# Performance work log

Hardware: AMD Instinct MI355X
Metric: run time of the kernel (lower is better)

Reference implementation:

```python
import jax, jax.numpy as jnp
import numpy as np

# ---- constants matching the torch module / entmax normmax_bisect defaults ----
ALPHA = 5.0                 # normmax alpha (entmax normmax_bisect default)
N_BISECT = 50               # bisection iterations
K_EXP = 1.0 / (ALPHA - 1.0)        # p_i propto (z_i - tau)_+^{1/(alpha-1)}
AK_EXP = ALPHA / (ALPHA - 1.0)     # norm condition: sum (z-tau)_+^{alpha/(alpha-1)} = 1
EPS = 1e-8                  # module epsilon
LN_EPS = 1e-5               # torch LayerNorm default eps

B, N, C, D = 32, 1024, 64, 768


def _bisect_tau(z):
    # z: [..., S]; find tau with f(tau) = sum_i relu(z_i - tau)^AK_EXP - 1 = 0 (f decreasing)
    max_val = jnp.max(z, axis=-1, keepdims=True)
    lo, hi = max_val - 1.0, max_val  # f(lo) >= 0, f(hi) = -1 < 0

    def body(_, carry):
        lo, hi = carry
        tau = 0.5 * (lo + hi)
        f = jnp.sum(jnp.maximum(z - tau, 0.0) ** AK_EXP, axis=-1, keepdims=True) - 1.0
        lo = jnp.where(f >= 0, tau, lo)
        hi = jnp.where(f >= 0, hi, tau)
        return (lo, hi)

    lo, hi = jax.lax.fori_loop(0, N_BISECT, body, (lo, hi))
    return 0.5 * (lo + hi)


def normmax_last(z):
    # normmax over last axis: p = s / sum(s), s = relu(z - tau)^{1/(alpha-1)}, ||s||_alpha = 1
    tau = _bisect_tau(z)
    u = jnp.maximum(z - tau, 0.0)
    u_safe = jnp.where(u > 0, u, 1.0)
    s = jnp.where(u > 0, u_safe ** K_EXP, 0.0)
    return s / jnp.sum(s, axis=-1, keepdims=True)


def layernorm(x, scale, bias):
    mu = jnp.mean(x, axis=-1, keepdims=True)
    var = jnp.mean((x - mu) ** 2, axis=-1, keepdims=True)
    return (x - mu) * jax.lax.rsqrt(var + LN_EPS) * scale + bias


def setup_inputs() -> dict:
    key = jax.random.key(0)
    ks = jax.random.split(key, 10)
    w = lambda k, shp: (jax.random.normal(k, shp, dtype=jnp.float32) * 0.02)
    return {
        "features": jax.random.normal(ks[0], (B, N, D), dtype=jnp.float32),
        "slots_init": jax.random.normal(ks[1], (B, C, D), dtype=jnp.float32),
        "mask": jax.random.randint(ks[2], (B, N), 0, 2, dtype=jnp.int32),
        "ln_f_scale": jnp.ones((D,), jnp.float32),
        "ln_f_bias": jnp.zeros((D,), jnp.float32),
        "ln_s_scale": jnp.ones((D,), jnp.float32),
        "ln_s_bias": jnp.zeros((D,), jnp.float32),
        "Wk": w(ks[3], (D, D)),
        "Wv": w(ks[4], (D, D)),
        "Wq": w(ks[5], (D, D)),
        "W_ih": w(ks[6], (3 * D, D)),
        "W_hh": w(ks[7], (3 * D, D)),
        "b_ih": jnp.zeros((3 * D,), jnp.float32),
        "b_hh": jnp.zeros((3 * D,), jnp.float32),
    }


def reference(features, slots_init, mask, ln_f_scale, ln_f_bias, ln_s_scale, ln_s_bias,
              Wk, Wv, Wq, W_ih, W_hh, b_ih, b_hh):
    f = layernorm(features, ln_f_scale, ln_f_bias)        # [B,N,D]
    k = f @ Wk.T
    v = f @ Wv.T
    b, n, d = v.shape
    c = slots_init.shape[1]
    m = mask[:, None, :] != 0                             # [B,1,N], broadcasts over C

    # num_iterations = 1; straight-through (detach trick) is the identity here.
    slots_prev = slots_init
    s = layernorm(slots_init, ln_s_scale, ln_s_bias)
    q = s @ Wq.T                                          # [B,C,D]
    logits = jnp.einsum('bcd,bnd->bcn', q, k) * (1.0 / np.sqrt(d))
    logits = jnp.where(m, logits, 0.0)                    # masked_fill(mask==0, 0)
    # normmax over the slot axis (dim=1)
    attn = jnp.moveaxis(normmax_last(jnp.moveaxis(logits, 1, -1)), -1, 1)  # [B,C,N]
    attn = jnp.where(m, attn, 0.0)
    attn_wm = attn / (jnp.sum(attn, axis=-1, keepdims=True) + EPS)
    updates = jnp.einsum('bcn,bnd->bcd', attn_wm, v)      # [B,C,D]

    # torch GRUCell: r,z,n gate order
    x = updates.reshape(-1, d)
    h = slots_prev.reshape(-1, d)
    gi = x @ W_ih.T + b_ih
    gh = h @ W_hh.T + b_hh
    ir, iz, in_ = jnp.split(gi, 3, axis=-1)
    hr, hz, hn = jnp.split(gh, 3, axis=-1)
    r = jax.nn.sigmoid(ir + hr)
    zg = jax.nn.sigmoid(iz + hz)
    ng = jnp.tanh(in_ + r * hn)
    h_new = (1.0 - zg) * ng + zg * h
    slots = h_new.reshape(b, c, d)
    return slots, attn
```

## Files before the change

kernel.cpp:

```cpp
#include <hip/hip_runtime.h>
#include <cstdint>
#include <cmath>

#define DEVINL __device__ __forceinline__


using f32x4  = __attribute__((ext_vector_type(4))) float;
using bf16x8 = __attribute__((ext_vector_type(8))) __bf16;
using u16x8  = __attribute__((ext_vector_type(8))) unsigned short;
using u16x4  = __attribute__((ext_vector_type(4))) unsigned short;
using fl4    = __attribute__((ext_vector_type(4))) float;

DEVINL float bf2f(unsigned short h) {
    unsigned int u = ((unsigned int)h) << 16;
    float f; __builtin_memcpy(&f, &u, 4); return f;
}
DEVINL unsigned short f2bf(float f) {
    unsigned int u; __builtin_memcpy(&u, &f, 4);
    u += 0x7FFFu + ((u >> 16) & 1u);
    return (unsigned short)(u >> 16);
}
DEVINL float sqrt_raw(float x) {
    float r; asm("v_sqrt_f32 %0, %1" : "=v"(r) : "v"(x)); return r;
}

DEVINL void gload_lds16(const unsigned short* g, unsigned short* l) {
    __builtin_amdgcn_global_load_lds(
        (__attribute__((address_space(1))) void*)g,
        (__attribute__((address_space(3))) void*)l,
        16, 0, 0);
}

__global__ __launch_bounds__(256)
void mask_scan(const int* __restrict__ mask, int* __restrict__ idx,
               int* __restrict__ cnt, int* __restrict__ cpad)
{
    constexpr int NB = 1024;
    const int b = blockIdx.x * 4 + (threadIdx.x >> 6);
    const int lane = threadIdx.x & 63;
    if (b >= 32) return;
    const int* mrow = mask + b * NB;
    int loc[16]; int lsum = 0;
#pragma unroll
    for (int i = 0; i < 16; ++i) { loc[i] = mrow[lane * 16 + i] != 0; lsum += loc[i]; }
    int pre = lsum;
#pragma unroll
    for (int o = 1; o < 64; o <<= 1) {
        int t = __shfl_up(pre, o);
        if (lane >= o) pre += t;
    }
    const int total = __shfl(pre, 63);
    pre -= lsum;
    int* ib = idx + b * NB;
    int p = pre;
#pragma unroll
    for (int i = 0; i < 16; ++i) if (loc[i]) ib[p++] = lane * 16 + i;
    if (lane == 0) {
        cnt[b] = total;
        int cp = (total + 63) & ~63;
        cpad[b] = cp < 64 ? 64 : cp;
    }
}

__global__ __launch_bounds__(256)
void zfill(float* __restrict__ p, int n4)
{
    const int i = blockIdx.x * 256 + threadIdx.x;
    if (i < n4) { fl4 z = {0.f, 0.f, 0.f, 0.f}; *(fl4*)(p + i * 4) = z; }
}

__global__ __launch_bounds__(256)
void tr2_f2b_split(const float* __restrict__ Wq, const float* __restrict__ Wk,
                   unsigned short* __restrict__ WqT_i, unsigned short* __restrict__ WkT_i)
{
    constexpr int S = 768 * 768;
    const int o = blockIdx.x * 256 + threadIdx.x;
    if (o >= 2 * S) return;
    const float* x; unsigned short* y; int i;
    if (o < S) { x = Wq; y = WqT_i; i = o; }
    else       { x = Wk; y = WkT_i; i = o - S; }
    const int e = i / 768, d = i - e * 768;
    const float v = x[d * 768 + e];
    const unsigned short h = f2bf(v);
    y[(long)e * 1536 + d]       = h;
    y[(long)e * 1536 + 768 + d] = f2bf(v - bf2f(h));
}

__global__ __launch_bounds__(256)
void conv2_fused(const float* __restrict__ Wih, const float* __restrict__ Whh,
                 const float* __restrict__ sl,  const float* __restrict__ Wv,
                 unsigned short* __restrict__ Wihb, unsigned short* __restrict__ Whhb,
                 unsigned short* __restrict__ slb,  unsigned short* __restrict__ Wvb)
{
    constexpr int S1 = 3 * 768 * 768;
    constexpr int S2 = S1 + 3 * 768 * 768;
    constexpr int S3 = S2 + 32 * 64 * 768;
    constexpr int S4 = S3 + 768 * 768;
    const int i = (blockIdx.x * 256 + threadIdx.x) * 4;
    if (i >= S4) return;
    const float* src; unsigned short* dst; int off;
    if (i < S1)      { src = Wih; dst = Wihb; off = i; }
    else if (i < S2) { src = Whh; dst = Whhb; off = i - S1; }
    else if (i < S3) { src = sl;  dst = slb;  off = i - S2; }
    else             { src = Wv;  dst = Wvb;  off = i - S3; }
    fl4 v = *(const fl4*)(src + off);
    u16x4 o;
#pragma unroll
    for (int j = 0; j < 4; ++j) o[j] = f2bf(v[j]);
    *(u16x4*)(dst + off) = o;
}

template<int BM, int BN, int WAVES_M, int WAVES_N, int OUTMODE>
__global__ __launch_bounds__(256)
void gemm_bt3(const unsigned short* __restrict__ AB, const unsigned short* __restrict__ BB,
              void* __restrict__ out1, const int* __restrict__ cpad,
              int N, int K, long sA, long sB, long sC, float alpha)
{
    constexpr int BK = 32;
    constexpr int WM = BM / WAVES_M, WN = BN / WAVES_N;
    constexpr int MT = WM / 16, NT = WN / 16;
    __shared__ alignas(16) unsigned short Ash[BM * BK], Asl[BM * BK];
    __shared__ alignas(16) unsigned short Bsh[BN * BK], Bsl[BN * BK];

    const int bz = blockIdx.z;
    const int row0 = blockIdx.y * BM, col0 = blockIdx.x * BN;
    if (cpad && col0 >= cpad[bz]) return;
    AB += (long)bz * sA;
    BB += (long)bz * sB;
    const int tid = threadIdx.x, l = tid & 63, w = tid >> 6;
    const int wm = w / WAVES_N, wn = w % WAVES_N;
    const int fr = l & 15, fq = l >> 4;

    f32x4 acc[MT][NT] = {};
    constexpr int ACALLS = (BM * BK) / (256 * 8);
    constexpr int BCALLS = (BN * BK) / (256 * 8);

    for (int kt = 0; kt < K; kt += BK) {
#pragma unroll
        for (int c = 0; c < ACALLS; ++c) {
            const int e = (c * 256 + tid) * 8;
            const long rb = (long)(row0 + (e >> 5)) * (2 * K) + kt + (e & 31);
            gload_lds16(AB + rb, &Ash[e]);
            gload_lds16(AB + rb + K, &Asl[e]);
        }
#pragma unroll
        for (int c = 0; c < BCALLS; ++c) {
            const int e = (c * 256 + tid) * 8;
            const long rb = (long)(col0 + (e >> 5)) * (2 * K) + kt + (e & 31);
            gload_lds16(BB + rb, &Bsh[e]);
            gload_lds16(BB + rb + K, &Bsl[e]);
        }
        __syncthreads();

        bf16x8 afh[MT], afl[MT], bfh[NT], bfl[NT];
#pragma unroll
        for (int m = 0; m < MT; ++m) {
            const int o = (wm * WM + m * 16 + fr) * BK + fq * 8;
            afh[m] = __builtin_bit_cast(bf16x8, *(const u16x8*)&Ash[o]);
            afl[m] = __builtin_bit_cast(bf16x8, *(const u16x8*)&Asl[o]);
        }
#pragma unroll
        for (int n = 0; n < NT; ++n) {
            const int o = (wn * WN + n * 16 + fr) * BK + fq * 8;
            bfh[n] = __builtin_bit_cast(bf16x8, *(const u16x8*)&Bsh[o]);
            bfl[n] = __builtin_bit_cast(bf16x8, *(const u16x8*)&Bsl[o]);
        }
#pragma unroll
        for (int m = 0; m < MT; ++m)
#pragma unroll
            for (int n = 0; n < NT; ++n) {
                acc[m][n] = __builtin_amdgcn_mfma_f32_16x16x32_bf16(afh[m], bfh[n], acc[m][n], 0, 0, 0);
                acc[m][n] = __builtin_amdgcn_mfma_f32_16x16x32_bf16(afh[m], bfl[n], acc[m][n], 0, 0, 0);
                acc[m][n] = __builtin_amdgcn_mfma_f32_16x16x32_bf16(afl[m], bfh[n], acc[m][n], 0, 0, 0);
            }
        __syncthreads();
    }

#pragma unroll
    for (int m = 0; m < MT; ++m) {
        const int gr = row0 + wm * WM + m * 16 + fq * 4;
#pragma unroll
        for (int n = 0; n < NT; ++n) {
            const int gc = col0 + wn * WN + n * 16 + fr;
#pragma unroll
            for (int j = 0; j < 4; ++j) {
                const float v = acc[m][n][j] * alpha;
                if (OUTMODE == 0) {
                    ((float*)out1)[(long)bz * sC + (long)(gr + j) * N + gc] = v;
                } else {
                    unsigned short* ob = (unsigned short*)out1;
                    const long rb = (long)(gr + j) * (2 * N) + gc;
                    const unsigned short h = f2bf(v);
                    ob[rb] = h;
                    ob[rb + N] = f2bf(v - bf2f(h));
                }
            }
        }
    }
}

template<int BM, int BN, int WAVES_M, int WAVES_N, bool OUT_F32>
__global__ __launch_bounds__(256)
void gemm_bt(const unsigned short* __restrict__ A,
             const unsigned short* __restrict__ B,
             void* __restrict__ Cv,
             int N, int K, long sA, long sB, long sC, float alpha)
{
    constexpr int BK = 32;
    constexpr int WM = BM / WAVES_M, WN = BN / WAVES_N;
    constexpr int MT = WM / 16, NT = WN / 16;
    __shared__ alignas(16) unsigned short As[BM * BK];
    __shared__ alignas(16) unsigned short Bs[BN * BK];

    const int bz = blockIdx.z;
    A += (long)bz * sA;
    B += (long)bz * sB;
    const int row0 = blockIdx.y * BM, col0 = blockIdx.x * BN;
    const int tid = threadIdx.x, l = tid & 63, w = tid >> 6;
    const int wm = w / WAVES_N, wn = w % WAVES_N;
    const int fr = l & 15, fq = l >> 4;

    f32x4 acc[MT][NT] = {};
    constexpr int ACALLS = (BM * BK) / (256 * 8);
    constexpr int BCALLS = (BN * BK) / (256 * 8);

    for (int kt = 0; kt < K; kt += BK) {
#pragma unroll
        for (int c = 0; c < ACALLS; ++c) {
            const int e = (c * 256 + tid) * 8;
            gload_lds16(A + (long)(row0 + (e >> 5)) * K + kt + (e & 31), &As[e]);
        }
#pragma unroll
        for (int c = 0; c < BCALLS; ++c) {
            const int e = (c * 256 + tid) * 8;
            gload_lds16(B + (long)(col0 + (e >> 5)) * K + kt + (e & 31), &Bs[e]);
        }
        __syncthreads();

        bf16x8 af[MT], bfr[NT];
#pragma unroll
        for (int m = 0; m < MT; ++m)
            af[m] = __builtin_bit_cast(bf16x8, *(const u16x8*)&As[(wm * WM + m * 16 + fr) * BK + fq * 8]);
#pragma unroll
        for (int n = 0; n < NT; ++n)
            bfr[n] = __builtin_bit_cast(bf16x8, *(const u16x8*)&Bs[(wn * WN + n * 16 + fr) * BK + fq * 8]);
#pragma unroll
        for (int m = 0; m < MT; ++m)
#pragma unroll
            for (int n = 0; n < NT; ++n)
                acc[m][n] = __builtin_amdgcn_mfma_f32_16x16x32_bf16(af[m], bfr[n], acc[m][n], 0, 0, 0);
        __syncthreads();
    }

#pragma unroll
    for (int m = 0; m < MT; ++m) {
        const int gr = row0 + wm * WM + m * 16 + fq * 4;
#pragma unroll
        for (int n = 0; n < NT; ++n) {
            const int gc = col0 + wn * WN + n * 16 + fr;
#pragma unroll
            for (int j = 0; j < 4; ++j) {
                const float v = acc[m][n][j] * alpha;
                if (OUT_F32) ((float*)Cv)[(long)bz * sC + (long)(gr + j) * N + gc] = v;
                else ((unsigned short*)Cv)[(long)bz * sC + (long)(gr + j) * N + gc] = f2bf(v);
            }
        }
    }
}

template<int BM, int BN, int WAVES_M, int WAVES_N>
__global__ __launch_bounds__(256)
void gemm_nt_rs(const unsigned short* __restrict__ A,
                const unsigned short* __restrict__ Bm,
                unsigned short* __restrict__ C,
                const int* __restrict__ cpad,
                int N, int Kmax, long sA, long sB, long sC)
{
    constexpr int BK = 32;
    constexpr int WM = BM / WAVES_M, WN = BN / WAVES_N;
    constexpr int MT = WM / 16, NT = WN / 16;
    __shared__ alignas(16) unsigned short As[BM * BK];
    __shared__ alignas(16) unsigned short Bs[BN * BK];
    __shared__ float rsums[BM];

    const int bz = blockIdx.z;
    const int Keff = cpad[bz];
    A += (long)bz * sA;
    Bm += (long)bz * sB;
    const int row0 = blockIdx.y * BM, col0 = blockIdx.x * BN;
    const int tid = threadIdx.x, l = tid & 63, w = tid >> 6;
    const int wm = w / WAVES_N, wn = w % WAVES_N;
    const int fr = l & 15, fq = l >> 4;

    f32x4 acc[MT][NT] = {};
    float rsum = 0.f;
    constexpr int ACALLS = (BM * BK) / (256 * 8);
    constexpr int TPR = BN / 8;
    constexpr int RPP = 256 / TPR;
    const int br = tid / TPR, bc8 = (tid % TPR) * 8;

    for (int kt = 0; kt < Keff; kt += BK) {
#pragma unroll
        for (int c = 0; c < ACALLS; ++c) {
            const int e = (c * 256 + tid) * 8;
            gload_lds16(A + (long)(row0 + (e >> 5)) * Kmax + kt + (e & 31), &As[e]);
        }
#pragma unroll
        for (int p = 0; p < BK / RPP; ++p) {
            const int r = p * RPP + br;
            u16x8 vv = *(const u16x8*)(Bm + (long)(kt + r) * (2 * N) + col0 + bc8);
#pragma unroll
            for (int j = 0; j < 8; ++j) Bs[(bc8 + j) * BK + r] = vv[j];
        }
        __syncthreads();

        if (tid < BM) {
#pragma unroll
            for (int kk = 0; kk < BK / 8; ++kk) {
                u16x8 vv = *(const u16x8*)&As[tid * BK + kk * 8];
#pragma unroll
                for (int j = 0; j < 8; ++j) rsum += bf2f(vv[j]);
            }
        }

        bf16x8 af[MT], bfr[NT];
#pragma unroll
        for (int m = 0; m < MT; ++m)
            af[m] = __builtin_bit_cast(bf16x8, *(const u16x8*)&As[(wm * WM + m * 16 + fr) * BK + fq * 8]);
#pragma unroll
        for (int n = 0; n < NT; ++n)
            bfr[n] = __builtin_bit_cast(bf16x8, *(const u16x8*)&Bs[(wn * WN + n * 16 + fr) * BK + fq * 8]);
#pragma unroll
        for (int m = 0; m < MT; ++m)
#pragma unroll
            for (int n = 0; n < NT; ++n)
                acc[m][n] = __builtin_amdgcn_mfma_f32_16x16x32_bf16(af[m], bfr[n], acc[m][n], 0, 0, 0);
        __syncthreads();
    }

    if (tid < BM) rsums[tid] = rsum;
    __syncthreads();

#pragma unroll
    for (int m = 0; m < MT; ++m) {
        const int lr = wm * WM + m * 16 + fq * 4;
        const int gr = row0 + lr;
#pragma unroll
        for (int n = 0; n < NT; ++n) {
            const int gc = col0 + wn * WN + n * 16 + fr;
#pragma unroll
            for (int j = 0; j < 4; ++j) {
                const float inv = 1.f / (rsums[lr + j] + 1e-8f);
                C[(long)bz * sC + (long)(gr + j) * N + gc] = f2bf(acc[m][n][j] * inv);
            }
        }
    }
}

__global__ __launch_bounds__(256)
void ln_fused_c(const float* __restrict__ xf, const float* __restrict__ gf,
                const float* __restrict__ bf,
                unsigned short* __restrict__ fi,
                const float* __restrict__ xs, const float* __restrict__ gs,
                const float* __restrict__ bs,
                unsigned short* __restrict__ si,
                const int* __restrict__ idx, const int* __restrict__ cnt,
                const int* __restrict__ cpad, int nrows_f)
{
    constexpr int D = 768;
    const int lane = threadIdx.x & 63;
    long row = (long)blockIdx.x * 4 + (threadIdx.x >> 6);
    const float *x, *g, *bb_;
    unsigned short* y;
    long srow;
    if (row < nrows_f) {
        const int b = (int)(row >> 10), j = (int)(row & 1023);
        if (j >= cpad[b]) return;
        y = fi; srow = row;
        unsigned short* yr = y + srow * (2 * D);
        if (j >= cnt[b]) {
            u16x8 z = {};
            unsigned short* p = yr + lane * 24;
            *(u16x8*)p = z; *(u16x8*)(p + 8) = z; *(u16x8*)(p + 16) = z;
            return;
        }
        const int n = idx[(b << 10) + j];
        x = xf + ((long)(b << 10) + n) * D;
        g = gf; bb_ = bf;
    } else {
        srow = row - nrows_f;
        x = xs + srow * D;
        g = gs; bb_ = bs; y = si;
    }

    const int eA = lane * 8;
    const int eB = 512 + lane * 8;
    float v[16];
    {
        fl4 a = *(const fl4*)(x + eA);
        fl4 b = *(const fl4*)(x + eA + 4);
#pragma unroll
        for (int j = 0; j < 4; ++j) { v[j] = a[j]; v[4 + j] = b[j]; }
    }
    if (lane < 32) {
        fl4 a = *(const fl4*)(x + eB);
        fl4 b = *(const fl4*)(x + eB + 4);
#pragma unroll
        for (int j = 0; j < 4; ++j) { v[8 + j] = a[j]; v[12 + j] = b[j]; }
    }
    float s = 0.f, s2 = 0.f;
#pragma unroll
    for (int j = 0; j < 8; ++j) { s += v[j]; s2 += v[j] * v[j]; }
    if (lane < 32) {
#pragma unroll
        for (int j = 8; j < 16; ++j) { s += v[j]; s2 += v[j] * v[j]; }
    }
#pragma unroll
    for (int o = 1; o < 64; o <<= 1) { s += __shfl_xor(s, o); s2 += __shfl_xor(s2, o); }
    const float mu  = s / (float)D;
    const float var = s2 / (float)D - mu * mu;
    const float r   = rsqrtf(var + 1e-5f);

    unsigned short* yr = (row < nrows_f ? fi : si) + srow * (2 * D);
    {
        fl4 g0 = *(const fl4*)(g + eA), g1 = *(const fl4*)(g + eA + 4);
        fl4 b0 = *(const fl4*)(bb_ + eA), b1 = *(const fl4*)(bb_ + eA + 4);
        u16x8 oh, ol;
#pragma unroll
        for (int j = 0; j < 8; ++j) {
            const float gg = (j < 4) ? g0[j] : g1[j - 4];
            const float be = (j < 4) ? b0[j] : b1[j - 4];
            const float yv = (v[j] - mu) * r * gg + be;
            oh[j] = f2bf(yv);
            ol[j] = f2bf(yv - bf2f(oh[j]));
        }
        *(u16x8*)(yr + eA) = oh;
        *(u16x8*)(yr + D + eA) = ol;
    }
    if (lane < 32) {
        fl4 g0 = *(const fl4*)(g + eB), g1 = *(const fl4*)(g + eB + 4);
        fl4 b0 = *(const fl4*)(bb_ + eB), b1 = *(const fl4*)(bb_ + eB + 4);
        u16x8 oh, ol;
#pragma unroll
        for (int j = 0; j < 8; ++j) {
            const float gg = (j < 4) ? g0[j] : g1[j - 4];
            const float be = (j < 4) ? b0[j] : b1[j - 4];
            const float yv = (v[8 + j] - mu) * r * gg + be;
            oh[j] = f2bf(yv);
            ol[j] = f2bf(yv - bf2f(oh[j]));
        }
        *(u16x8*)(yr + eB) = oh;
        *(u16x8*)(yr + D + eB) = ol;
    }
}

__global__ __launch_bounds__(256)
void normmax_cols_c(const float* __restrict__ logits,
                    const int* __restrict__ idx, const int* __restrict__ cnt,
                    const int* __restrict__ cpad,
                    float* __restrict__ attn_f32, unsigned short* __restrict__ attn_b16)
{
    constexpr int N = 1024, C = 64;
    const int b = blockIdx.y;
    const int j0 = blockIdx.x * 64;
    if (j0 >= cpad[b]) return;
    const int tid = threadIdx.x, l = tid & 63, w = tid >> 6;
    const int j = j0 + w * 16 + (l & 15);
    const int cb = (l >> 4) * 16;
    const long base = (long)b * C * N + j;
    const bool valid = j < cnt[b];

    float z[16];
#pragma unroll
    for (int i = 0; i < 16; ++i) z[i] = valid ? logits[base + (long)(cb + i) * N] : 0.f;

    float mx = z[0];
#pragma unroll
    for (int i = 1; i < 16; ++i) mx = fmaxf(mx, z[i]);
    mx = fmaxf(mx, __shfl_xor(mx, 16));
    mx = fmaxf(mx, __shfl_xor(mx, 32));

    float lo = mx - 1.f, hi = mx;
    for (int it = 0; it < 34; ++it) {
        const float tau = 0.5f * (lo + hi);
        float f = 0.f;
#pragma unroll
        for (int i = 0; i < 16; ++i) {
            const float u = fmaxf(z[i] - tau, 0.f);
            f += u * sqrt_raw(sqrt_raw(u));
        }
        f += __shfl_xor(f, 16);
        f += __shfl_xor(f, 32);
        if (f >= 1.f) lo = tau; else hi = tau;
    }
    const float tau = 0.5f * (lo + hi);
    float sv[16]; float ss = 0.f;
#pragma unroll
    for (int i = 0; i < 16; ++i) {
        const float u = fmaxf(z[i] - tau, 0.f);
        sv[i] = sqrt_raw(sqrt_raw(u));
        ss += sv[i];
    }
    ss += __shfl_xor(ss, 16);
    ss += __shfl_xor(ss, 32);
    const float inv = 1.f / ss;
    const int n = valid ? idx[(b << 10) + j] : 0;
#pragma unroll
    for (int i = 0; i < 16; ++i) {
        const float a = valid ? sv[i] * inv : 0.f;
        attn_b16[base + (long)(cb + i) * N] = f2bf(a);
        if (valid) attn_f32[(long)b * C * N + (long)(cb + i) * N + n] = a;
    }
}

__global__ __launch_bounds__(256)
void gru_gates(const float* __restrict__ gi, const float* __restrict__ gh,
               const float* __restrict__ b_ih, const float* __restrict__ b_hh,
               const float* __restrict__ h, float* __restrict__ out)
{
    constexpr int D = 768;
    const int t = blockIdx.x * 256 + threadIdx.x;
    const int row = t / (D / 4), d = (t - row * (D / 4)) * 4;
    const float* gir = gi + (long)row * 3 * D;
    const float* ghr = gh + (long)row * 3 * D;
    fl4 ir  = *(const fl4*)(gir + d);
    fl4 iz  = *(const fl4*)(gir + D + d);
    fl4 in_ = *(const fl4*)(gir + 2 * D + d);
    fl4 hr  = *(const fl4*)(ghr + d);
    fl4 hz  = *(const fl4*)(ghr + D + d);
    fl4 hn  = *(const fl4*)(ghr + 2 * D + d);
    fl4 bir = *(const fl4*)(b_ih + d);
    fl4 biz = *(const fl4*)(b_ih + D + d);
    fl4 bin = *(const fl4*)(b_ih + 2 * D + d);
    fl4 bhr = *(const fl4*)(b_hh + d);
    fl4 bhz = *(const fl4*)(b_hh + D + d);
    fl4 bhn = *(const fl4*)(b_hh + 2 * D + d);
    fl4 hv  = *(const fl4*)(h + (long)row * D + d);
    fl4 o;
#pragma unroll
    for (int j = 0; j < 4; ++j) {
        const float r  = 1.f / (1.f + expf(-(ir[j] + bir[j] + hr[j] + bhr[j])));
        const float zg = 1.f / (1.f + expf(-(iz[j] + biz[j] + hz[j] + bhz[j])));
        const float ng = tanhf(in_[j] + bin[j] + r * (hn[j] + bhn[j]));
        o[j] = (1.f - zg) * ng + zg * hv[j];
    }
    *(fl4*)(out + (long)row * D + d) = o;
}

extern "C" void kernel_launch(void* const* d_in, const int* in_sizes, int n_in,
                              void* d_out, int out_size, void* d_ws, size_t ws_size,
                              hipStream_t stream)
{
    const float* features = (const float*)d_in[0];
    const float* slots    = (const float*)d_in[1];
    const int*   mask     = (const int*)d_in[2];
    const float* lnf_g = (const float*)d_in[3];
    const float* lnf_b = (const float*)d_in[4];
    const float* lns_g = (const float*)d_in[5];
    const float* lns_b = (const float*)d_in[6];
    const float* Wk  = (const float*)d_in[7];
    const float* Wv  = (const float*)d_in[8];
    const float* Wq  = (const float*)d_in[9];
    const float* Wih = (const float*)d_in[10];
    const float* Whh = (const float*)d_in[11];
    const float* bih = (const float*)d_in[12];
    const float* bhh = (const float*)d_in[13];

    constexpr int B = 32, N = 1024, C = 64, D = 768;
    char* ws = (char*)d_ws;
    unsigned short* f_i  = (unsigned short*)(ws + 0);
    float*          gi   = (float*)(ws + 0);
    float*          gh   = (float*)(ws + 18874368);
    unsigned short* Wihb = (unsigned short*)(ws + 37748736);
    unsigned short* Whhb = (unsigned short*)(ws + 41287680);
    unsigned short* Wvb  = (unsigned short*)(ws + 44826624);
    unsigned short* updb = (unsigned short*)(ws + 57671680);
    unsigned short* slb  = (unsigned short*)(ws + 60817408);
    float*          lg     = (float*)(ws + 100663296);
    unsigned short* s_i    = (unsigned short*)(ws + 109051904);
    unsigned short* ab16   = (unsigned short*)(ws + 109051904);
    unsigned short* qk_i   = (unsigned short*)(ws + 115343360);
    unsigned short* Pbf    = (unsigned short*)(ws + 115343360);
    unsigned short* WqT_i  = (unsigned short*)(ws + 121634816);
    unsigned short* WkT_i  = (unsigned short*)(ws + 123994112);
    unsigned short* M_i    = (unsigned short*)(ws + 126353408);
    int*            idx    = (int*)(ws + 128712704);
    int*            cnt    = (int*)(ws + 128843776);
    int*            cpad   = (int*)(ws + 128843904);

    float* out_slots = (float*)d_out;
    float* out_attn  = out_slots + (long)B * C * D;

    mask_scan<<<8, 256, 0, stream>>>(mask, idx, cnt, cpad);
    zfill<<<(B * C * N / 4 + 255) / 256, 256, 0, stream>>>(out_attn, B * C * N / 4);

    tr2_f2b_split<<<(2 * D * D + 255) / 256, 256, 0, stream>>>(Wq, Wk, WqT_i, WkT_i);

    ln_fused_c<<<(B * N + B * C) / 4, 256, 0, stream>>>(
        features, lnf_g, lnf_b, f_i,
        slots, lns_g, lns_b, s_i,
        idx, cnt, cpad, B * N);

    gemm_bt3<64, 64, 2, 2, 1><<<dim3(D / 64, D / 64, 1), 256, 0, stream>>>(
        WkT_i, WqT_i, M_i, nullptr, D, D, 0, 0, 0, 1.f);
    gemm_bt3<64, 64, 2, 2, 1><<<dim3(D / 64, (B * C) / 64, 1), 256, 0, stream>>>(
        s_i, M_i, qk_i, nullptr, D, D, 0, 0, 0, 1.f);
    gemm_bt3<64, 64, 2, 2, 0><<<dim3(N / 64, 1, B), 256, 0, stream>>>(
        qk_i, f_i, lg, cpad,
        N, D, (long)C * 2 * D, (long)N * 2 * D, (long)C * N, 0.03608439182435161f);

    normmax_cols_c<<<dim3(N / 64, B), 256, 0, stream>>>(lg, idx, cnt, cpad, out_attn, ab16);

    gemm_nt_rs<64, 64, 2, 2><<<dim3(D / 64, 1, B), 256, 0, stream>>>(
        ab16, f_i, Pbf, cpad, D, N, (long)C * N, (long)N * 2 * D, (long)C * D);

    {
        constexpr int TOT = 3 * D * D + 3 * D * D + B * C * D + D * D;
        conv2_fused<<<(TOT / 4 + 255) / 256, 256, 0, stream>>>(
            Wih, Whh, slots, Wv, Wihb, Whhb, slb, Wvb);
    }

    gemm_bt<64, 64, 2, 2, false><<<dim3(D / 64, (B * C) / 64, 1), 256, 0, stream>>>(
        Pbf, Wvb, updb, D, D, 0, 0, 0, 1.f);

    gemm_bt<128, 128, 2, 2, true><<<dim3(3 * D / 128, (B * C) / 128, 2), 256, 0, stream>>>(
        updb, Wihb, gi, 3 * D, D,
        (long)(B * C) * D, (long)(3 * D) * D, (long)(B * C) * 3 * D, 1.f);

    gru_gates<<<(B * C * D / 4) / 256, 256, 0, stream>>>(gi, gh, bih, bhh, slots, out_slots);
}
```

Baseline: 202.4 us.

## Fuse GRU input/hidden GEMMs with gate epilogue; merge mask scan and zero-fill

Replaces the batched GRU GEMM, which wrote gi/gh to fp32 workspace, and the separate gates kernel with one kernel. Each 64x64 output tile computes all three gate projections for both input and hidden paths and applies the GRU nonlinearity in registers. Mask scan and attention zero-fill are also merged into one launch. This removes the large gi/gh round trip through memory and two launches, but the new GEMM is single-buffered with a 64x64 tile and holds many accumulators, which may lower occupancy.

```diff
diff --git a/kernel.cpp b/kernel.cpp
--- a/kernel.cpp
+++ b/kernel.cpp
@@ -32,11 +32,18 @@
 }
 
 __global__ __launch_bounds__(256)
-void mask_scan(const int* __restrict__ mask, int* __restrict__ idx,
-               int* __restrict__ cnt, int* __restrict__ cpad)
-{
+void mask_scan_zfill(const int* __restrict__ mask, int* __restrict__ idx,
+                     int* __restrict__ cnt, int* __restrict__ cpad,
+                     float* __restrict__ zp)
+{
+    if (blockIdx.x < 2048) {
+        const int i = blockIdx.x * 256 + threadIdx.x;
+        fl4 z = {0.f, 0.f, 0.f, 0.f};
+        *(fl4*)(zp + (long)i * 4) = z;
+        return;
+    }
     constexpr int NB = 1024;
-    const int b = blockIdx.x * 4 + (threadIdx.x >> 6);
+    const int b = (blockIdx.x - 2048) * 4 + (threadIdx.x >> 6);
     const int lane = threadIdx.x & 63;
     if (b >= 32) return;
     const int* mrow = mask + b * NB;
@@ -60,13 +67,6 @@
         int cp = (total + 63) & ~63;
         cpad[b] = cp < 64 ? 64 : cp;
     }
-}
-
-__global__ __launch_bounds__(256)
-void zfill(float* __restrict__ p, int n4)
-{
-    const int i = blockIdx.x * 256 + threadIdx.x;
-    if (i < n4) { fl4 z = {0.f, 0.f, 0.f, 0.f}; *(fl4*)(p + i * 4) = z; }
 }
 
 __global__ __launch_bounds__(256)
@@ -268,6 +268,87 @@
     }
 }
 
+__global__ __launch_bounds__(256)
+void gemm_gru(const unsigned short* __restrict__ updb, const unsigned short* __restrict__ slb,
+              const unsigned short* __restrict__ Wihb, const unsigned short* __restrict__ Whhb,
+              const float* __restrict__ b_ih, const float* __restrict__ b_hh,
+              const float* __restrict__ h, float* __restrict__ out)
+{
+    constexpr int BK = 32, Kd = 768, Dd = 768;
+    __shared__ alignas(16) unsigned short Au[64 * BK], As[64 * BK];
+    __shared__ alignas(16) unsigned short Bi[3][64 * BK], Bh[3][64 * BK];
+
+    const int row0 = blockIdx.y * 64, col0 = blockIdx.x * 64;
+    const int tid = threadIdx.x, l = tid & 63, w = tid >> 6;
+    const int wm = w >> 1, wn = w & 1;
+    const int fr = l & 15, fq = l >> 4;
+
+    f32x4 ai[3][2][2] = {}, ah[3][2][2] = {};
+
+    for (int kt = 0; kt < Kd; kt += BK) {
+        {
+            const int e = tid * 8;
+            const long rb = (long)(row0 + (e >> 5)) * Kd + kt + (e & 31);
+            gload_lds16(updb + rb, &Au[e]);
+            gload_lds16(slb + rb, &As[e]);
+#pragma unroll
+            for (int g = 0; g < 3; ++g) {
+                const long wb = (long)(g * Dd + col0 + (e >> 5)) * Kd + kt + (e & 31);
+                gload_lds16(Wihb + wb, &Bi[g][e]);
+                gload_lds16(Whhb + wb, &Bh[g][e]);
+            }
+        }
+        __syncthreads();
+
+        bf16x8 au[2], as_[2], bi[3][2], bh[3][2];
+#pragma unroll
+        for (int m = 0; m < 2; ++m) {
+            const int o = (wm * 32 + m * 16 + fr) * BK + fq * 8;
+            au[m]  = __builtin_bit_cast(bf16x8, *(const u16x8*)&Au[o]);
+            as_[m] = __builtin_bit_cast(bf16x8, *(const u16x8*)&As[o]);
+        }
+#pragma unroll
+        for (int n = 0; n < 2; ++n) {
+            const int o = (wn * 32 + n * 16 + fr) * BK + fq * 8;
+#pragma unroll
+            for (int g = 0; g < 3; ++g) {
+                bi[g][n] = __builtin_bit_cast(bf16x8, *(const u16x8*)&Bi[g][o]);
+                bh[g][n] = __builtin_bit_cast(bf16x8, *(const u16x8*)&Bh[g][o]);
+            }
+        }
+#pragma unroll
+        for (int g = 0; g < 3; ++g)
+#pragma unroll
+            for (int m = 0; m < 2; ++m)
+#pragma unroll
+                for (int n = 0; n < 2; ++n) {
+                    ai[g][m][n] = __builtin_amdgcn_mfma_f32_16x16x32_bf16(au[m],  bi[g][n], ai[g][m][n], 0, 0, 0);
+                    ah[g][m][n] = __builtin_amdgcn_mfma_f32_16x16x32_bf16(as_[m], bh[g][n], ah[g][m][n], 0, 0, 0);
+                }
+        __syncthreads();
+    }
+
+#pragma unroll
+    for (int m = 0; m < 2; ++m) {
+        const int gr = row0 + wm * 32 + m * 16 + fq * 4;
+#pragma unroll
+        for (int n = 0; n < 2; ++n) {
+            const int gc = col0 + wn * 32 + n * 16 + fr;
+            const float bir = b_ih[gc],        bhr = b_hh[gc];
+            const float biz = b_ih[Dd + gc],   bhz = b_hh[Dd + gc];
+            const float bin = b_ih[2*Dd + gc], bhn = b_hh[2*Dd + gc];
+#pragma unroll
+            for (int j = 0; j < 4; ++j) {
+                const float r  = 1.f / (1.f + expf(-(ai[0][m][n][j] + bir + ah[0][m][n][j] + bhr)));
+                const float zg = 1.f / (1.f + expf(-(ai[1][m][n][j] + biz + ah[1][m][n][j] + bhz)));
+                const float ng = tanhf(ai[2][m][n][j] + bin + r * (ah[2][m][n][j] + bhn));
+                const long idx = (long)(gr + j) * Dd + gc;
+                out[idx] = (1.f - zg) * ng + zg * h[idx];
+            }
+        }
+    }
+}
+
 template<int BM, int BN, int WAVES_M, int WAVES_N>
 __global__ __launch_bounds__(256)
 void gemm_nt_rs(const unsigned short* __restrict__ A,
@@ -371,13 +452,12 @@
     const int lane = threadIdx.x & 63;
     long row = (long)blockIdx.x * 4 + (threadIdx.x >> 6);
     const float *x, *g, *bb_;
-    unsigned short* y;
     long srow;
     if (row < nrows_f) {
         const int b = (int)(row >> 10), j = (int)(row & 1023);
         if (j >= cpad[b]) return;
-        y = fi; srow = row;
-        unsigned short* yr = y + srow * (2 * D);
+        srow = row;
+        unsigned short* yr = fi + srow * (2 * D);
         if (j >= cnt[b]) {
             u16x8 z = {};
             unsigned short* p = yr + lane * 24;
@@ -390,7 +470,7 @@
     } else {
         srow = row - nrows_f;
         x = xs + srow * D;
-        g = gs; bb_ = bs; y = si;
+        g = gs; bb_ = bs;
     }
 
     const int eA = lane * 8;
@@ -511,40 +591,6 @@
         attn_b16[base + (long)(cb + i) * N] = f2bf(a);
         if (valid) attn_f32[(long)b * C * N + (long)(cb + i) * N + n] = a;
     }
-}
-
-__global__ __launch_bounds__(256)
-void gru_gates(const float* __restrict__ gi, const float* __restrict__ gh,
-               const float* __restrict__ b_ih, const float* __restrict__ b_hh,
-               const float* __restrict__ h, float* __restrict__ out)
-{
-    constexpr int D = 768;
-    const int t = blockIdx.x * 256 + threadIdx.x;
-    const int row = t / (D / 4), d = (t - row * (D / 4)) * 4;
-    const float* gir = gi + (long)row * 3 * D;
-    const float* ghr = gh + (long)row * 3 * D;
-    fl4 ir  = *(const fl4*)(gir + d);
-    fl4 iz  = *(const fl4*)(gir + D + d);
-    fl4 in_ = *(const fl4*)(gir + 2 * D + d);
-    fl4 hr  = *(const fl4*)(ghr + d);
-    fl4 hz  = *(const fl4*)(ghr + D + d);
-    fl4 hn  = *(const fl4*)(ghr + 2 * D + d);
-    fl4 bir = *(const fl4*)(b_ih + d);
-    fl4 biz = *(const fl4*)(b_ih + D + d);
-    fl4 bin = *(const fl4*)(b_ih + 2 * D + d);
-    fl4 bhr = *(const fl4*)(b_hh + d);
-    fl4 bhz = *(const fl4*)(b_hh + D + d);
-    fl4 bhn = *(const fl4*)(b_hh + 2 * D + d);
-    fl4 hv  = *(const fl4*)(h + (long)row * D + d);
-    fl4 o;
-#pragma unroll
-    for (int j = 0; j < 4; ++j) {
-        const float r  = 1.f / (1.f + expf(-(ir[j] + bir[j] + hr[j] + bhr[j])));
-        const float zg = 1.f / (1.f + expf(-(iz[j] + biz[j] + hz[j] + bhz[j])));
-        const float ng = tanhf(in_[j] + bin[j] + r * (hn[j] + bhn[j]));
-        o[j] = (1.f - zg) * ng + zg * hv[j];
-    }
-    *(fl4*)(out + (long)row * D + d) = o;
 }
 
 extern "C" void kernel_launch(void* const* d_in, const int* in_sizes, int n_in,
@@ -569,8 +615,6 @@
     constexpr int B = 32, N = 1024, C = 64, D = 768;
     char* ws = (char*)d_ws;
     unsigned short* f_i  = (unsigned short*)(ws + 0);
-    float*          gi   = (float*)(ws + 0);
-    float*          gh   = (float*)(ws + 18874368);
     unsigned short* Wihb = (unsigned short*)(ws + 37748736);
     unsigned short* Whhb = (unsigned short*)(ws + 41287680);
     unsigned short* Wvb  = (unsigned short*)(ws + 44826624);
@@ -591,8 +635,7 @@
     float* out_slots = (float*)d_out;
     float* out_attn  = out_slots + (long)B * C * D;
 
-    mask_scan<<<8, 256, 0, stream>>>(mask, idx, cnt, cpad);
-    zfill<<<(B * C * N / 4 + 255) / 256, 256, 0, stream>>>(out_attn, B * C * N / 4);
+    mask_scan_zfill<<<2056, 256, 0, stream>>>(mask, idx, cnt, cpad, out_attn);
 
     tr2_f2b_split<<<(2 * D * D + 255) / 256, 256, 0, stream>>>(Wq, Wk, WqT_i, WkT_i);
 
@@ -623,9 +666,6 @@
     gemm_bt<64, 64, 2, 2, false><<<dim3(D / 64, (B * C) / 64, 1), 256, 0, stream>>>(
         Pbf, Wvb, updb, D, D, 0, 0, 0, 1.f);
 
-    gemm_bt<128, 128, 2, 2, true><<<dim3(3 * D / 128, (B * C) / 128, 2), 256, 0, stream>>>(
-        updb, Wihb, gi, 3 * D, D,
-        (long)(B * C) * D, (long)(3 * D) * D, (long)(B * C) * 3 * D, 1.f);
-
-    gru_gates<<<(B * C * D / 4) / 256, 256, 0, stream>>>(gi, gh, bih, bhh, slots, out_slots);
-}
+    gemm_gru<<<dim3(D / 64, (B * C) / 64), 256, 0, stream>>>(
+        updb, slb, Wihb, Whhb, bih, bhh, slots, out_slots);
+}
```

Result: faster. 197.4 us (-2.5%).
